# Optimization experiments

Measured on AMD Instinct MI355X. Metric: run time of the kernel, lower is better.

The kernel has to match this reference:

```python
import jax, jax.numpy as jnp
import numpy as np
import math

C = 512
B, T = 8, 2048
STRIDE = 2
LN_EPS = 1e-5
EPS = 1e-8


def _ln(x, g, b):
    mu = jnp.mean(x, axis=-1, keepdims=True)
    var = jnp.mean(jnp.square(x - mu), axis=-1, keepdims=True)
    return (x - mu) * jax.lax.rsqrt(var + LN_EPS) * g + b


def _lin(x, w, b):
    # torch Linear: y = x @ W^T + b, W: [out, in]
    return jnp.einsum('btc,oc->bto', x, w) + b


def setup_inputs() -> dict:
    key = jax.random.key(0)
    ks = iter(jax.random.split(key, 40))
    s = 0.02
    d = {'x': jax.random.normal(next(ks), (B, T, C), jnp.float32)}
    # downsample conv: [C_out, C_in, K]
    d['dw'] = jax.random.normal(next(ks), (C, C, 3), jnp.float32) * s
    d['db'] = jnp.zeros((C,), jnp.float32)
    for br in ('cr', 'd', 'c'):
        for p in ('q', 'k', 'v'):
            d[f'w{p}_{br}'] = jax.random.normal(next(ks), (C, C), jnp.float32) * s
            d[f'b{p}_{br}'] = jnp.zeros((C,), jnp.float32)
        d[f'ln_{br}_g'] = jnp.ones((C,), jnp.float32)
        d[f'ln_{br}_b'] = jnp.zeros((C,), jnp.float32)
    d['temp'] = jnp.asarray(0.1, jnp.float32)
    d['gw'] = jax.random.normal(next(ks), (3, 3 * C), jnp.float32) * s  # conv1d k=1 squeezed
    d['gb'] = jnp.zeros((3,), jnp.float32)
    return d


def _forward(x, dw, db, wq_cr, bq_cr, wk_cr, bk_cr, wv_cr, bv_cr, ln_cr_g, ln_cr_b,
             wq_d, bq_d, wk_d, bk_d, wv_d, bv_d, ln_d_g, ln_d_b,
             wq_c, bq_c, wk_c, bk_c, wv_c, bv_c, ln_c_g, ln_c_b,
             temp, gw, gb):
    scale = 1.0 / math.sqrt(C)
    # downsample: Conv1d(k=3, stride, pad=1) on [B,C,T]
    xc = jnp.transpose(x, (0, 2, 1))
    xd = jax.lax.conv_general_dilated(
        xc, dw, window_strides=(STRIDE,), padding=[(1, 1)],
        dimension_numbers=('NCH', 'OIH', 'NCH')) + db[None, :, None]
    x_down = jnp.transpose(xd, (0, 2, 1))  # [B, T//2, C]

    # cross-resolution branch
    q = _lin(x, wq_cr, bq_cr)
    k = _lin(x_down, wk_cr, bk_cr)
    v = _lin(x_down, wv_cr, bv_cr)
    a = jax.nn.softmax(jnp.einsum('btc,bsc->bts', q, k) * scale, axis=-1)
    out_cross = _ln(jnp.einsum('bts,bsc->btc', a, v), ln_cr_g, ln_cr_b)

    # dot-product branch
    q = _lin(x, wq_d, bq_d)
    k = _lin(x, wk_d, bk_d)
    v = _lin(x, wv_d, bv_d)
    a = jax.nn.softmax(jnp.einsum('btc,bsc->bts', q, k) * scale, axis=-1)
    out_dot = _ln(jnp.einsum('bts,bsc->btc', a, v), ln_d_g, ln_d_b)

    # cosine branch with learnable temperature
    q = _lin(x, wq_c, bq_c)
    k = _lin(x, wk_c, bk_c)
    qn = q / (jnp.linalg.norm(q, axis=2, keepdims=True) + EPS)
    kn = k / (jnp.linalg.norm(k, axis=2, keepdims=True) + EPS)
    t = jnp.maximum(temp, 0.01)
    a = jax.nn.softmax(jnp.einsum('btc,bsc->bts', qn, kn) / t, axis=-1)
    v = _lin(x, wv_c, bv_c)
    out_cos = _ln(jnp.einsum('bts,bsc->btc', a, v), ln_c_g, ln_c_b)

    # learned gating fusion (conv1d k=1 == per-position linear over 3C)
    fused = jnp.concatenate([out_cross, out_dot, out_cos], axis=-1)  # [B,T,3C]
    gate = jax.nn.softmax(jnp.einsum('btc,gc->btg', fused, gw) + gb, axis=-1)  # [B,T,3]
    z = (gate[..., 0:1] * out_cross + gate[..., 1:2] * out_dot + gate[..., 2:3] * out_cos)
    return z


def reference(x, dw, db, wq_cr, bq_cr, wk_cr, bk_cr, wv_cr, bv_cr, ln_cr_g, ln_cr_b,
              wq_d, bq_d, wk_d, bk_d, wv_d, bv_d, ln_d_g, ln_d_b,
              wq_c, bq_c, wk_c, bk_c, wv_c, bv_c, ln_c_g, ln_c_b,
              temp, gw, gb):
    return _forward(x, dw, db, wq_cr, bq_cr, wk_cr, bk_cr, wv_cr, bv_cr, ln_cr_g, ln_cr_b,
                    wq_d, bq_d, wk_d, bk_d, wv_d, bv_d, ln_d_g, ln_d_b,
                    wq_c, bq_c, wk_c, bk_c, wv_c, bv_c, ln_c_g, ln_c_b,
                    temp, gw, gb)
```

## Files before the change

### kernel.cpp

```cpp
#include <hip/hip_runtime.h>


typedef __attribute__((ext_vector_type(8))) __bf16 bf16x8;
typedef __attribute__((ext_vector_type(4))) float f32x4;

#define CDIM 512
#define TFULL 2048

#define GLL16(gp, lp)                                                        \
  __builtin_amdgcn_global_load_lds(                                          \
      (const __attribute__((address_space(1))) unsigned int*)(gp),           \
      (__attribute__((address_space(3))) unsigned int*)(lp), 16, 0, 0)

__device__ __forceinline__ unsigned short f2bf(float f) {
  unsigned u = __float_as_uint(f);
  u = (u + 0x7fffu + ((u >> 16) & 1u)) >> 16;
  return (unsigned short)u;
}
__device__ __forceinline__ float bf2f(unsigned short h) {
  return __uint_as_float(((unsigned)h) << 16);
}

__global__ __launch_bounds__(256)
void k_tobf16(const float* __restrict__ src, unsigned short* __restrict__ dst, long n4) {
  long i = (long)blockIdx.x * 256 + threadIdx.x;
  if (i >= n4) return;
  float4 f = reinterpret_cast<const float4*>(src)[i];
  unsigned short o4[4] = {f2bf(f.x), f2bf(f.y), f2bf(f.z), f2bf(f.w)};
  reinterpret_cast<uint2*>(dst)[i] = *reinterpret_cast<const uint2*>(o4);
}

__global__ __launch_bounds__(256)
void k_dwreorder(const float* __restrict__ dw, unsigned short* __restrict__ dwb) {
  int idx = blockIdx.x * 256 + threadIdx.x;
  if (idx >= 512 * 1536) return;
  int o = idx / 1536, rem = idx - o * 1536;
  int k = rem >> 9, i = rem & 511;
  dwb[idx] = f2bf(dw[(o * 512 + i) * 3 + k]);
}

__global__ __launch_bounds__(256)
void k_im2col(const float* __restrict__ x, unsigned short* __restrict__ aim) {
  long idx = (long)blockIdx.x * 256 + threadIdx.x;
  if (idx >= (long)8192 * 1536 / 4) return;
  long e = idx * 4;
  int row = (int)(e / 1536);
  int col = (int)(e - (long)row * 1536);
  int b = row >> 10, t = row & 1023;
  int k = col >> 9, i = col & 511;
  int r = 2 * t - 1 + k;
  float4 f = {0.f, 0.f, 0.f, 0.f};
  if (r >= 0) f = *reinterpret_cast<const float4*>(x + ((long)b * TFULL + r) * CDIM + i);
  unsigned short o4[4] = {f2bf(f.x), f2bf(f.y), f2bf(f.z), f2bf(f.w)};
  *reinterpret_cast<uint2*>(aim + e) = *reinterpret_cast<const uint2*>(o4);
}

__global__ __launch_bounds__(256)
void k_gemm(const unsigned short* __restrict__ A,
            const unsigned short* __restrict__ B,
            void* __restrict__ Cp,
            int K, int lda, int ldb, int ldc,
            long sA, long sB, long sC,
            const float* __restrict__ bias,
            float alpha, const float* __restrict__ tempPtr,
            int mode, int ldct) {
  const int gx = gridDim.x;
  const int nwg = gx * gridDim.y;
  int wg = blockIdx.x + gx * blockIdx.y;
  wg = (wg & 7) * (nwg >> 3) + (wg >> 3);
  const int tm0 = (wg % gx) * 128, tn0 = (wg / gx) * 128;
  const int bz = blockIdx.z;
  const unsigned short* Ag = A + (long)bz * sA;
  const unsigned short* Bg = B + (long)bz * sB;

  __shared__ __align__(16) unsigned short smem[32768];

  const int tid = threadIdx.x;
  const int lane = tid & 63;
  const int wave = tid >> 6;
  const int wm = (wave >> 1) * 64, wn = (wave & 1) * 64;
  const int lrow = lane & 15, kq = lane >> 4;

  f32x4 acc[4][4];
#pragma unroll
  for (int i = 0; i < 4; ++i)
#pragma unroll
    for (int j = 0; j < 4; ++j) acc[i][j] = f32x4{0.f, 0.f, 0.f, 0.f};

  const int sr = tid >> 3;
  const int sj = (tid & 7) ^ (sr & 7);
  const unsigned short* aSrc = Ag + (long)(tm0 + sr) * lda + sj * 8;
  const unsigned short* bSrc = Bg + (long)(tn0 + sr) * ldb + sj * 8;

  const int nt = K >> 6;

#define STAGE(kt_, buf_)                                                     \
  {                                                                          \
    unsigned short* aD = smem + (buf_) * 8192 + wave * 512;                  \
    unsigned short* bD = smem + 16384 + (buf_) * 8192 + wave * 512;          \
    _Pragma("unroll")                                                        \
    for (int rd = 0; rd < 4; ++rd) {                                         \
      GLL16(aSrc + (kt_) + (long)rd * 32 * lda, aD + rd * 2048);             \
      GLL16(bSrc + (kt_) + (long)rd * 32 * ldb, bD + rd * 2048);             \
    }                                                                        \
  }

  STAGE(0, 0);

  const int xr = (lrow & 7) << 3;
  for (int t = 0; t < nt; ++t) {
    __syncthreads();
    if (t + 1 < nt) STAGE((t + 1) << 6, (t + 1) & 1);
    const unsigned short* As_ = smem + (t & 1) * 8192;
    const unsigned short* Bs_ = smem + 16384 + (t & 1) * 8192;
    bf16x8 af[4][2], bfv[4][2];
#pragma unroll
    for (int mi = 0; mi < 4; ++mi)
#pragma unroll
      for (int ks = 0; ks < 2; ++ks)
        af[mi][ks] = *reinterpret_cast<const bf16x8*>(
            &As_[(wm + mi * 16 + lrow) * 64 + ((ks * 32 + kq * 8) ^ xr)]);
#pragma unroll
    for (int ni = 0; ni < 4; ++ni)
#pragma unroll
      for (int ks = 0; ks < 2; ++ks)
        bfv[ni][ks] = *reinterpret_cast<const bf16x8*>(
            &Bs_[(wn + ni * 16 + lrow) * 64 + ((ks * 32 + kq * 8) ^ xr)]);
#pragma unroll
    for (int mi = 0; mi < 4; ++mi)
#pragma unroll
      for (int ni = 0; ni < 4; ++ni) {
        acc[mi][ni] = __builtin_amdgcn_mfma_f32_16x16x32_bf16(af[mi][0], bfv[ni][0], acc[mi][ni], 0, 0, 0);
        acc[mi][ni] = __builtin_amdgcn_mfma_f32_16x16x32_bf16(af[mi][1], bfv[ni][1], acc[mi][ni], 0, 0, 0);
      }
  }
#undef STAGE

  if (tempPtr) alpha = 1.0f / fmaxf(*tempPtr, 0.01f);

  if (mode == 1) {
    unsigned short* Cb = (unsigned short*)Cp + (long)bz * sC;
#pragma unroll
    for (int mi = 0; mi < 4; ++mi) {
      int rg = tm0 + wm + mi * 16 + kq * 4;
#pragma unroll
      for (int ni = 0; ni < 4; ++ni) {
        int cg = tn0 + wn + ni * 16 + lrow;
        float bb = bias ? bias[cg] : 0.f;
        f32x4 v = acc[mi][ni];
#pragma unroll
        for (int r = 0; r < 4; ++r)
          Cb[(long)(rg + r) * ldc + cg] = f2bf(v[r] * alpha + bb);
      }
    }
  } else {
    unsigned short* Cb = (unsigned short*)Cp + (long)bz * sC;
#pragma unroll
    for (int mi = 0; mi < 4; ++mi) {
      int rg = tm0 + wm + mi * 16 + kq * 4;
#pragma unroll
      for (int ni = 0; ni < 4; ++ni) {
        int cg = tn0 + wn + ni * 16 + lrow;
        float bb = bias ? bias[cg] : 0.f;
        f32x4 v = acc[mi][ni];
#pragma unroll
        for (int r = 0; r < 4; ++r)
          Cb[(long)cg * ldct + (rg + r)] = f2bf(v[r] * alpha + bb);
      }
    }
  }
}

__global__ __launch_bounds__(256)
void k_softmax(unsigned short* __restrict__ S, int cols) {
  const long base = (long)blockIdx.x * cols;
  const int tid = threadIdx.x, lane = tid & 63, wave = tid >> 6;
  const int nv = cols >> 3;
  float f[8];
  float mx = -3.0e38f;
  if (tid < nv) {
    uint4 v = *reinterpret_cast<const uint4*>(S + base + tid * 8);
    const unsigned short* pv = (const unsigned short*)&v;
#pragma unroll
    for (int j = 0; j < 8; ++j) { f[j] = bf2f(pv[j]); mx = fmaxf(mx, f[j]); }
  }
  __shared__ float rmax[4], rsum[4];
#pragma unroll
  for (int o = 32; o > 0; o >>= 1) mx = fmaxf(mx, __shfl_down(mx, o));
  if (lane == 0) rmax[wave] = mx;
  __syncthreads();
  mx = fmaxf(fmaxf(rmax[0], rmax[1]), fmaxf(rmax[2], rmax[3]));
  float sum = 0.f;
  if (tid < nv) {
#pragma unroll
    for (int j = 0; j < 8; ++j) { f[j] = __expf(f[j] - mx); sum += f[j]; }
  }
#pragma unroll
  for (int o = 32; o > 0; o >>= 1) sum += __shfl_down(sum, o);
  if (lane == 0) rsum[wave] = sum;
  __syncthreads();
  const float inv = 1.0f / (rsum[0] + rsum[1] + rsum[2] + rsum[3]);
  if (tid < nv) {
    unsigned short o8[8];
#pragma unroll
    for (int j = 0; j < 8; ++j) o8[j] = f2bf(f[j] * inv);
    *reinterpret_cast<uint4*>(S + base + tid * 8) = *reinterpret_cast<const uint4*>(o8);
  }
}

__global__ __launch_bounds__(256)
void k_l2norm(unsigned short* __restrict__ Q) {
  const int lane = threadIdx.x & 63, wave = threadIdx.x >> 6;
  const long row = (long)blockIdx.x * 4 + wave;
  unsigned short* p = Q + row * CDIM + lane * 8;
  uint4 v = *reinterpret_cast<const uint4*>(p);
  const unsigned short* pv = (const unsigned short*)&v;
  float f[8]; float q = 0.f;
#pragma unroll
  for (int j = 0; j < 8; ++j) { f[j] = bf2f(pv[j]); q += f[j] * f[j]; }
#pragma unroll
  for (int o = 32; o > 0; o >>= 1) q += __shfl_xor(q, o);
  float sc = 1.0f / (sqrtf(q) + 1e-8f);
  unsigned short o8[8];
#pragma unroll
  for (int j = 0; j < 8; ++j) o8[j] = f2bf(f[j] * sc);
  *reinterpret_cast<uint4*>(p) = *reinterpret_cast<const uint4*>(o8);
}

__global__ __launch_bounds__(256)
void k_ln_bf(unsigned short* __restrict__ X, const float* __restrict__ g,
             const float* __restrict__ b) {
  const int lane = threadIdx.x & 63, wave = threadIdx.x >> 6;
  const long row = (long)blockIdx.x * 4 + wave;
  unsigned short* p = X + row * CDIM + lane * 8;
  uint4 v = *reinterpret_cast<const uint4*>(p);
  const unsigned short* pv = (const unsigned short*)&v;
  float f[8];
  float s = 0.f, q = 0.f;
#pragma unroll
  for (int j = 0; j < 8; ++j) { f[j] = bf2f(pv[j]); s += f[j]; q += f[j] * f[j]; }
#pragma unroll
  for (int o = 32; o > 0; o >>= 1) { s += __shfl_xor(s, o); q += __shfl_xor(q, o); }
  float mu = s * (1.f / 512.f);
  float var = q * (1.f / 512.f) - mu * mu;
  float rs = rsqrtf(var + 1e-5f);
  float gg[8], bb[8];
  *reinterpret_cast<float4*>(&gg[0]) = *reinterpret_cast<const float4*>(g + lane * 8);
  *reinterpret_cast<float4*>(&gg[4]) = *reinterpret_cast<const float4*>(g + lane * 8 + 4);
  *reinterpret_cast<float4*>(&bb[0]) = *reinterpret_cast<const float4*>(b + lane * 8);
  *reinterpret_cast<float4*>(&bb[4]) = *reinterpret_cast<const float4*>(b + lane * 8 + 4);
  unsigned short o8[8];
#pragma unroll
  for (int j = 0; j < 8; ++j) o8[j] = f2bf((f[j] - mu) * rs * gg[j] + bb[j]);
  *reinterpret_cast<uint4*>(p) = *reinterpret_cast<const uint4*>(o8);
}

__global__ __launch_bounds__(256)
void k_gate(const unsigned short* __restrict__ o0, const unsigned short* __restrict__ o1,
            const unsigned short* __restrict__ o2, const float* __restrict__ gw,
            const float* __restrict__ gb, float* __restrict__ out) {
  __shared__ float gws[3 * 1536];
  for (int i = threadIdx.x; i < 3 * 1536; i += 256) gws[i] = gw[i];
  __syncthreads();
  const int lane = threadIdx.x & 63, wave = threadIdx.x >> 6;
  const long pos = (long)blockIdx.x * 4 + wave;
  const long off = pos * CDIM + lane * 8;
  float a[8], bq[8], cq[8];
  {
    uint4 va = *reinterpret_cast<const uint4*>(o0 + off);
    uint4 vb = *reinterpret_cast<const uint4*>(o1 + off);
    uint4 vc = *reinterpret_cast<const uint4*>(o2 + off);
    const unsigned short* pa = (const unsigned short*)&va;
    const unsigned short* pb = (const unsigned short*)&vb;
    const unsigned short* pc = (const unsigned short*)&vc;
#pragma unroll
    for (int j = 0; j < 8; ++j) { a[j] = bf2f(pa[j]); bq[j] = bf2f(pb[j]); cq[j] = bf2f(pc[j]); }
  }
  float l0 = 0.f, l1 = 0.f, l2 = 0.f;
  const int ch = lane * 8;
#pragma unroll
  for (int j = 0; j < 8; ++j) {
    l0 += a[j] * gws[ch + j] + bq[j] * gws[512 + ch + j] + cq[j] * gws[1024 + ch + j];
    l1 += a[j] * gws[1536 + ch + j] + bq[j] * gws[2048 + ch + j] + cq[j] * gws[2560 + ch + j];
    l2 += a[j] * gws[3072 + ch + j] + bq[j] * gws[3584 + ch + j] + cq[j] * gws[4096 + ch + j];
  }
#pragma unroll
  for (int o = 32; o > 0; o >>= 1) {
    l0 += __shfl_xor(l0, o); l1 += __shfl_xor(l1, o); l2 += __shfl_xor(l2, o);
  }
  l0 += gb[0]; l1 += gb[1]; l2 += gb[2];
  float m = fmaxf(l0, fmaxf(l1, l2));
  float e0 = __expf(l0 - m), e1 = __expf(l1 - m), e2 = __expf(l2 - m);
  float inv = 1.f / (e0 + e1 + e2);
  float g0 = e0 * inv, g1 = e1 * inv, g2 = e2 * inv;
  float r[8];
#pragma unroll
  for (int j = 0; j < 8; ++j) r[j] = g0 * a[j] + g1 * bq[j] + g2 * cq[j];
  *reinterpret_cast<float4*>(out + off) = *reinterpret_cast<const float4*>(&r[0]);
  *reinterpret_cast<float4*>(out + off + 4) = *reinterpret_cast<const float4*>(&r[4]);
}

extern "C" void kernel_launch(void* const* d_in, const int* in_sizes, int n_in,
                              void* d_out, int out_size, void* d_ws, size_t ws_size,
                              hipStream_t stream) {
  (void)in_sizes; (void)n_in; (void)out_size;
  const float* x = (const float*)d_in[0];
  const float* dw = (const float*)d_in[1];
  const float* db = (const float*)d_in[2];
  const float* W[9] = {(const float*)d_in[3],  (const float*)d_in[5],  (const float*)d_in[7],
                       (const float*)d_in[11], (const float*)d_in[13], (const float*)d_in[15],
                       (const float*)d_in[19], (const float*)d_in[21], (const float*)d_in[23]};
  const float* bq_cr = (const float*)d_in[4];
  const float* bk_cr = (const float*)d_in[6];
  const float* bv_cr = (const float*)d_in[8];
  const float* ln_cr_g = (const float*)d_in[9];
  const float* ln_cr_b = (const float*)d_in[10];
  const float* bq_d = (const float*)d_in[12];
  const float* bk_d = (const float*)d_in[14];
  const float* bv_d = (const float*)d_in[16];
  const float* ln_d_g = (const float*)d_in[17];
  const float* ln_d_b = (const float*)d_in[18];
  const float* bq_c = (const float*)d_in[20];
  const float* bk_c = (const float*)d_in[22];
  const float* bv_c = (const float*)d_in[24];
  const float* ln_c_g = (const float*)d_in[25];
  const float* ln_c_b = (const float*)d_in[26];
  const float* temp = (const float*)d_in[27];
  const float* gw = (const float*)d_in[28];
  const float* gb = (const float*)d_in[29];

  if (ws_size < 230000000ULL) return;

  char* p = (char*)d_ws;
  auto alloc = [&](size_t bytes) {
    void* r = (void*)p;
    p += (bytes + 255) & ~(size_t)255;
    return r;
  };
  unsigned short* XB  = (unsigned short*)alloc(16384L * 512 * 2);
  unsigned short* XD  = (unsigned short*)alloc(8192L * 512 * 2);
  unsigned short* WB  = (unsigned short*)alloc(9L * 262144 * 2);
  unsigned short* DWB = (unsigned short*)alloc(512L * 1536 * 2);
  unsigned short* QB  = (unsigned short*)alloc(16384L * 512 * 2);
  unsigned short* KB  = (unsigned short*)alloc(16384L * 512 * 2);
  unsigned short* VTB = (unsigned short*)alloc(16384L * 512 * 2);
  unsigned short* OUT0 = (unsigned short*)alloc(16384L * 512 * 2);
  unsigned short* OUT1 = (unsigned short*)alloc(16384L * 512 * 2);
  unsigned short* OUT2 = (unsigned short*)alloc(16384L * 512 * 2);
  unsigned short* SB = (unsigned short*)alloc(8L * 2048 * 2048 * 2);
  unsigned short* AIM = SB;

  const float scale = 0.044194173824159216f;

  auto gemm = [&](const unsigned short* A, const unsigned short* Bm, void* Cm,
                  int M, int N, int K, int lda, int ldb, int ldc,
                  int batch, long sA, long sB, long sC,
                  const float* bias, float alpha, const float* tp, int mode, int ldct) {
    dim3 g(M / 128, N / 128, batch);
    k_gemm<<<g, 256, 0, stream>>>(A, Bm, Cm, K, lda, ldb, ldc, sA, sB, sC,
                                  bias, alpha, tp, mode, ldct);
  };

  k_tobf16<<<8192, 256, 0, stream>>>(x, XB, 16384L * 512 / 4);
  for (int j = 0; j < 9; ++j)
    k_tobf16<<<256, 256, 0, stream>>>(W[j], WB + j * 262144L, 65536);
  k_dwreorder<<<3072, 256, 0, stream>>>(dw, DWB);
  k_im2col<<<12288, 256, 0, stream>>>(x, AIM);

  gemm(AIM, DWB, XD, 8192, 512, 1536, 1536, 1536, 512, 1, 0, 0, 0,
       db, 1.f, nullptr, 1, 0);

  gemm(XB, WB + 0 * 262144L, QB, 16384, 512, 512, 512, 512, 512, 1, 0, 0, 0,
       bq_cr, 1.f, nullptr, 1, 0);
  gemm(XD, WB + 1 * 262144L, KB, 8192, 512, 512, 512, 512, 512, 1, 0, 0, 0,
       bk_cr, 1.f, nullptr, 1, 0);
  gemm(XD, WB + 2 * 262144L, VTB, 1024, 512, 512, 512, 512, 0, 8,
       1024L * 512, 0, 512L * 1024, bv_cr, 1.f, nullptr, 2, 1024);
  gemm(QB, KB, SB, 2048, 1024, 512, 512, 512, 1024, 8,
       2048L * 512, 1024L * 512, 2048L * 1024, nullptr, scale, nullptr, 1, 0);
  k_softmax<<<16384, 256, 0, stream>>>(SB, 1024);
  gemm(SB, VTB, OUT0, 2048, 512, 1024, 1024, 1024, 512, 8,
       2048L * 1024, 512L * 1024, 2048L * 512, nullptr, 1.f, nullptr, 1, 0);
  k_ln_bf<<<4096, 256, 0, stream>>>(OUT0, ln_cr_g, ln_cr_b);

  gemm(XB, WB + 3 * 262144L, QB, 16384, 512, 512, 512, 512, 512, 1, 0, 0, 0,
       bq_d, 1.f, nullptr, 1, 0);
  gemm(XB, WB + 4 * 262144L, KB, 16384, 512, 512, 512, 512, 512, 1, 0, 0, 0,
       bk_d, 1.f, nullptr, 1, 0);
  gemm(XB, WB + 5 * 262144L, VTB, 2048, 512, 512, 512, 512, 0, 8,
       2048L * 512, 0, 512L * 2048, bv_d, 1.f, nullptr, 2, 2048);
  gemm(QB, KB, SB, 2048, 2048, 512, 512, 512, 2048, 8,
       2048L * 512, 2048L * 512, 2048L * 2048, nullptr, scale, nullptr, 1, 0);
  k_softmax<<<16384, 256, 0, stream>>>(SB, 2048);
  gemm(SB, VTB, OUT1, 2048, 512, 2048, 2048, 2048, 512, 8,
       2048L * 2048, 512L * 2048, 2048L * 512, nullptr, 1.f, nullptr, 1, 0);
  k_ln_bf<<<4096, 256, 0, stream>>>(OUT1, ln_d_g, ln_d_b);

  gemm(XB, WB + 6 * 262144L, QB, 16384, 512, 512, 512, 512, 512, 1, 0, 0, 0,
       bq_c, 1.f, nullptr, 1, 0);
  gemm(XB, WB + 7 * 262144L, KB, 16384, 512, 512, 512, 512, 512, 1, 0, 0, 0,
       bk_c, 1.f, nullptr, 1, 0);
  k_l2norm<<<4096, 256, 0, stream>>>(QB);
  k_l2norm<<<4096, 256, 0, stream>>>(KB);
  gemm(XB, WB + 8 * 262144L, VTB, 2048, 512, 512, 512, 512, 0, 8,
       2048L * 512, 0, 512L * 2048, bv_c, 1.f, nullptr, 2, 2048);
  gemm(QB, KB, SB, 2048, 2048, 512, 512, 512, 2048, 8,
       2048L * 512, 2048L * 512, 2048L * 2048, nullptr, 1.f, temp, 1, 0);
  k_softmax<<<16384, 256, 0, stream>>>(SB, 2048);
  gemm(SB, VTB, OUT2, 2048, 512, 2048, 2048, 2048, 512, 8,
       2048L * 2048, 512L * 2048, 2048L * 512, nullptr, 1.f, nullptr, 1, 0);
  k_ln_bf<<<4096, 256, 0, stream>>>(OUT2, ln_c_g, ln_c_b);

  k_gate<<<4096, 256, 0, stream>>>(OUT0, OUT1, OUT2, gw, gb, (float*)d_out);
}
```

Measured before the change: 596.6 us.

## Add 256x256 GEMM for attention scores, fuse Q/K projections, batch weight casts

Adds a 512-thread GEMM kernel with 256x256 tiles, double-buffered direct-to-LDS loads and a workgroup swizzle, and uses it for the three QK^T score GEMMs. The Q and K projections of the dot and cosine branches are merged into one N=1024 GEMM that writes an interleaved QK buffer, with the biases packed by device copies. The nine weight bf16 conversions become a single launch. The aim is higher MFMA utilisation and less launch overhead, at the cost of a larger workspace, strided Q/K reads, and more register pressure in the new kernel.

```diff
diff --git a/kernel.cpp b/kernel.cpp
--- a/kernel.cpp
+++ b/kernel.cpp
@@ -28,6 +28,17 @@
   float4 f = reinterpret_cast<const float4*>(src)[i];
   unsigned short o4[4] = {f2bf(f.x), f2bf(f.y), f2bf(f.z), f2bf(f.w)};
   reinterpret_cast<uint2*>(dst)[i] = *reinterpret_cast<const uint2*>(o4);
+}
+
+struct WPtrs { const float* p[9]; };
+__global__ __launch_bounds__(256)
+void k_tobf16w(WPtrs w, unsigned short* __restrict__ dst) {
+  int idx = blockIdx.x * 256 + threadIdx.x;
+  if (idx >= 9 * 65536) return;
+  int m = idx >> 16, off = idx & 65535;
+  float4 f = reinterpret_cast<const float4*>(w.p[m])[off];
+  unsigned short o4[4] = {f2bf(f.x), f2bf(f.y), f2bf(f.z), f2bf(f.w)};
+  reinterpret_cast<uint2*>(dst + (long)m * 262144)[off] = *reinterpret_cast<const uint2*>(o4);
 }
 
 __global__ __launch_bounds__(256)
@@ -171,6 +182,103 @@
   }
 }
 
+__global__ __launch_bounds__(512)
+void k_gemm256(const unsigned short* __restrict__ A,
+               const unsigned short* __restrict__ B,
+               unsigned short* __restrict__ C,
+               int K, int lda, int ldb, int ldc,
+               long sA, long sB, long sC,
+               float alpha, const float* __restrict__ tempPtr) {
+  const int gx = gridDim.x;
+  const int nwg = gx * gridDim.y;
+  int wg = blockIdx.x + gx * blockIdx.y;
+  wg = (wg & 7) * (nwg >> 3) + (wg >> 3);
+  const int tm0 = (wg % gx) * 256, tn0 = (wg / gx) * 256;
+  const unsigned short* Ag = A + (long)blockIdx.z * sA;
+  const unsigned short* Bg = B + (long)blockIdx.z * sB;
+
+  __shared__ __align__(16) unsigned short smem[32768];
+
+  const int tid = threadIdx.x;
+  const int lane = tid & 63;
+  const int wave = tid >> 6;
+  const int wm = (wave >> 2) * 128, wn = (wave & 3) * 64;
+  const int lrow = lane & 15, kq = lane >> 4;
+
+  f32x4 acc[8][4];
+#pragma unroll
+  for (int i = 0; i < 8; ++i)
+#pragma unroll
+    for (int j = 0; j < 4; ++j) acc[i][j] = f32x4{0.f, 0.f, 0.f, 0.f};
+
+  const int srow = lane >> 2;
+  const int sslot = (lane & 3) ^ ((lane >> 3) & 3);
+  const unsigned short* aS0 = Ag + (long)(tm0 + wave * 16 + srow) * lda + sslot * 8;
+  const unsigned short* aS1 = aS0 + 128L * lda;
+  const unsigned short* bS0 = Bg + (long)(tn0 + wave * 16 + srow) * ldb + sslot * 8;
+  const unsigned short* bS1 = bS0 + 128L * ldb;
+
+  const int nt = K >> 5;
+
+#define STAGE256(kt_, buf_)                                                  \
+  {                                                                          \
+    unsigned short* aD = smem + (buf_) * 8192 + wave * 512;                  \
+    unsigned short* bD = smem + 16384 + (buf_) * 8192 + wave * 512;          \
+    GLL16(aS0 + (kt_), aD);                                                  \
+    GLL16(aS1 + (kt_), aD + 4096);                                           \
+    GLL16(bS0 + (kt_), bD);                                                  \
+    GLL16(bS1 + (kt_), bD + 4096);                                           \
+  }
+
+  STAGE256(0, 0);
+
+  const int xr = ((lrow >> 1) & 3) << 3;
+  for (int t = 0; t < nt; ++t) {
+    if (t + 1 < nt) {
+      STAGE256((t + 1) << 5, (t + 1) & 1);
+      asm volatile("s_waitcnt vmcnt(4)" ::: "memory");
+    } else {
+      asm volatile("s_waitcnt vmcnt(0)" ::: "memory");
+    }
+    __builtin_amdgcn_s_barrier();
+    __builtin_amdgcn_sched_barrier(0);
+    const unsigned short* As_ = smem + (t & 1) * 8192;
+    const unsigned short* Bs_ = smem + 16384 + (t & 1) * 8192;
+    bf16x8 bfv[4];
+#pragma unroll
+    for (int ni = 0; ni < 4; ++ni)
+      bfv[ni] = *reinterpret_cast<const bf16x8*>(
+          &Bs_[(wn + ni * 16 + lrow) * 32 + ((kq * 8) ^ xr)]);
+#pragma unroll
+    for (int mi = 0; mi < 8; ++mi) {
+      bf16x8 af = *reinterpret_cast<const bf16x8*>(
+          &As_[(wm + mi * 16 + lrow) * 32 + ((kq * 8) ^ xr)]);
+#pragma unroll
+      for (int ni = 0; ni < 4; ++ni)
+        acc[mi][ni] = __builtin_amdgcn_mfma_f32_16x16x32_bf16(af, bfv[ni], acc[mi][ni], 0, 0, 0);
+    }
+    __builtin_amdgcn_sched_barrier(0);
+    if (t + 1 < nt) __builtin_amdgcn_s_barrier();
+  }
+#undef STAGE256
+
+  if (tempPtr) alpha = 1.0f / fmaxf(*tempPtr, 0.01f);
+
+  C += (long)blockIdx.z * sC;
+#pragma unroll
+  for (int mi = 0; mi < 8; ++mi) {
+    int rg = tm0 + wm + mi * 16 + kq * 4;
+#pragma unroll
+    for (int ni = 0; ni < 4; ++ni) {
+      int cg = tn0 + wn + ni * 16 + lrow;
+      f32x4 v = acc[mi][ni];
+#pragma unroll
+      for (int r = 0; r < 4; ++r)
+        C[(long)(rg + r) * ldc + cg] = f2bf(v[r] * alpha);
+    }
+  }
+}
+
 __global__ __launch_bounds__(256)
 void k_softmax(unsigned short* __restrict__ S, int cols) {
   const long base = (long)blockIdx.x * cols;
@@ -209,10 +317,10 @@
 }
 
 __global__ __launch_bounds__(256)
-void k_l2norm(unsigned short* __restrict__ Q) {
+void k_l2norm(unsigned short* __restrict__ Q, int ld) {
   const int lane = threadIdx.x & 63, wave = threadIdx.x >> 6;
   const long row = (long)blockIdx.x * 4 + wave;
-  unsigned short* p = Q + row * CDIM + lane * 8;
+  unsigned short* p = Q + row * ld + lane * 8;
   uint4 v = *reinterpret_cast<const uint4*>(p);
   const unsigned short* pv = (const unsigned short*)&v;
   float f[8]; float q = 0.f;
@@ -307,9 +415,12 @@
   const float* x = (const float*)d_in[0];
   const float* dw = (const float*)d_in[1];
   const float* db = (const float*)d_in[2];
-  const float* W[9] = {(const float*)d_in[3],  (const float*)d_in[5],  (const float*)d_in[7],
-                       (const float*)d_in[11], (const float*)d_in[13], (const float*)d_in[15],
-                       (const float*)d_in[19], (const float*)d_in[21], (const float*)d_in[23]};
+  WPtrs wp;
+  wp.p[0] = (const float*)d_in[3];  wp.p[1] = (const float*)d_in[5];
+  wp.p[2] = (const float*)d_in[7];  wp.p[3] = (const float*)d_in[11];
+  wp.p[4] = (const float*)d_in[13]; wp.p[5] = (const float*)d_in[15];
+  wp.p[6] = (const float*)d_in[19]; wp.p[7] = (const float*)d_in[21];
+  wp.p[8] = (const float*)d_in[23];
   const float* bq_cr = (const float*)d_in[4];
   const float* bk_cr = (const float*)d_in[6];
   const float* bv_cr = (const float*)d_in[8];
@@ -329,7 +440,7 @@
   const float* gw = (const float*)d_in[28];
   const float* gb = (const float*)d_in[29];
 
-  if (ws_size < 230000000ULL) return;
+  if (ws_size < 240000000ULL) return;
 
   char* p = (char*)d_ws;
   auto alloc = [&](size_t bytes) {
@@ -342,11 +453,13 @@
   unsigned short* WB  = (unsigned short*)alloc(9L * 262144 * 2);
   unsigned short* DWB = (unsigned short*)alloc(512L * 1536 * 2);
   unsigned short* QB  = (unsigned short*)alloc(16384L * 512 * 2);
-  unsigned short* KB  = (unsigned short*)alloc(16384L * 512 * 2);
+  unsigned short* KB  = (unsigned short*)alloc(8192L * 512 * 2);
   unsigned short* VTB = (unsigned short*)alloc(16384L * 512 * 2);
   unsigned short* OUT0 = (unsigned short*)alloc(16384L * 512 * 2);
   unsigned short* OUT1 = (unsigned short*)alloc(16384L * 512 * 2);
   unsigned short* OUT2 = (unsigned short*)alloc(16384L * 512 * 2);
+  unsigned short* QK2 = (unsigned short*)alloc(16384L * 1024 * 2);
+  float* BC = (float*)alloc(2048 * 4);
   unsigned short* SB = (unsigned short*)alloc(8L * 2048 * 2048 * 2);
   unsigned short* AIM = SB;
 
@@ -360,12 +473,22 @@
     k_gemm<<<g, 256, 0, stream>>>(A, Bm, Cm, K, lda, ldb, ldc, sA, sB, sC,
                                   bias, alpha, tp, mode, ldct);
   };
+  auto gemm256 = [&](const unsigned short* A, const unsigned short* Bm,
+                     unsigned short* Cm, int M, int N, int K,
+                     int lda, int ldb, int ldc, int batch,
+                     long sA, long sB, long sC, float alpha, const float* tp) {
+    dim3 g(M / 256, N / 256, batch);
+    k_gemm256<<<g, 512, 0, stream>>>(A, Bm, Cm, K, lda, ldb, ldc, sA, sB, sC, alpha, tp);
+  };
 
   k_tobf16<<<8192, 256, 0, stream>>>(x, XB, 16384L * 512 / 4);
-  for (int j = 0; j < 9; ++j)
-    k_tobf16<<<256, 256, 0, stream>>>(W[j], WB + j * 262144L, 65536);
+  k_tobf16w<<<2304, 256, 0, stream>>>(wp, WB);
   k_dwreorder<<<3072, 256, 0, stream>>>(dw, DWB);
   k_im2col<<<12288, 256, 0, stream>>>(x, AIM);
+  hipMemcpyAsync(BC,        bq_d, 512 * 4, hipMemcpyDeviceToDevice, stream);
+  hipMemcpyAsync(BC + 512,  bk_d, 512 * 4, hipMemcpyDeviceToDevice, stream);
+  hipMemcpyAsync(BC + 1024, bq_c, 512 * 4, hipMemcpyDeviceToDevice, stream);
+  hipMemcpyAsync(BC + 1536, bk_c, 512 * 4, hipMemcpyDeviceToDevice, stream);
 
   gemm(AIM, DWB, XD, 8192, 512, 1536, 1536, 1536, 512, 1, 0, 0, 0,
        db, 1.f, nullptr, 1, 0);
@@ -376,36 +499,32 @@
        bk_cr, 1.f, nullptr, 1, 0);
   gemm(XD, WB + 2 * 262144L, VTB, 1024, 512, 512, 512, 512, 0, 8,
        1024L * 512, 0, 512L * 1024, bv_cr, 1.f, nullptr, 2, 1024);
-  gemm(QB, KB, SB, 2048, 1024, 512, 512, 512, 1024, 8,
-       2048L * 512, 1024L * 512, 2048L * 1024, nullptr, scale, nullptr, 1, 0);
+  gemm256(QB, KB, SB, 2048, 1024, 512, 512, 512, 1024, 8,
+          2048L * 512, 1024L * 512, 2048L * 1024, scale, nullptr);
   k_softmax<<<16384, 256, 0, stream>>>(SB, 1024);
   gemm(SB, VTB, OUT0, 2048, 512, 1024, 1024, 1024, 512, 8,
        2048L * 1024, 512L * 1024, 2048L * 512, nullptr, 1.f, nullptr, 1, 0);
   k_ln_bf<<<4096, 256, 0, stream>>>(OUT0, ln_cr_g, ln_cr_b);
 
-  gemm(XB, WB + 3 * 262144L, QB, 16384, 512, 512, 512, 512, 512, 1, 0, 0, 0,
-       bq_d, 1.f, nullptr, 1, 0);
-  gemm(XB, WB + 4 * 262144L, KB, 16384, 512, 512, 512, 512, 512, 1, 0, 0, 0,
-       bk_d, 1.f, nullptr, 1, 0);
+  gemm(XB, WB + 3 * 262144L, QK2, 16384, 1024, 512, 512, 512, 1024, 1, 0, 0, 0,
+       BC, 1.f, nullptr, 1, 0);
   gemm(XB, WB + 5 * 262144L, VTB, 2048, 512, 512, 512, 512, 0, 8,
        2048L * 512, 0, 512L * 2048, bv_d, 1.f, nullptr, 2, 2048);
-  gemm(QB, KB, SB, 2048, 2048, 512, 512, 512, 2048, 8,
-       2048L * 512, 2048L * 512, 2048L * 2048, nullptr, scale, nullptr, 1, 0);
+  gemm256(QK2, QK2 + 512, SB, 2048, 2048, 512, 1024, 1024, 2048, 8,
+          2048L * 1024, 2048L * 1024, 2048L * 2048, scale, nullptr);
   k_softmax<<<16384, 256, 0, stream>>>(SB, 2048);
   gemm(SB, VTB, OUT1, 2048, 512, 2048, 2048, 2048, 512, 8,
        2048L * 2048, 512L * 2048, 2048L * 512, nullptr, 1.f, nullptr, 1, 0);
   k_ln_bf<<<4096, 256, 0, stream>>>(OUT1, ln_d_g, ln_d_b);
 
-  gemm(XB, WB + 6 * 262144L, QB, 16384, 512, 512, 512, 512, 512, 1, 0, 0, 0,
-       bq_c, 1.f, nullptr, 1, 0);
-  gemm(XB, WB + 7 * 262144L, KB, 16384, 512, 512, 512, 512, 512, 1, 0, 0, 0,
-       bk_c, 1.f, nullptr, 1, 0);
-  k_l2norm<<<4096, 256, 0, stream>>>(QB);
-  k_l2norm<<<4096, 256, 0, stream>>>(KB);
+  gemm(XB, WB + 6 * 262144L, QK2, 16384, 1024, 512, 512, 512, 1024, 1, 0, 0, 0,
+       BC + 1024, 1.f, nullptr, 1, 0);
+  k_l2norm<<<4096, 256, 0, stream>>>(QK2, 1024);
+  k_l2norm<<<4096, 256, 0, stream>>>(QK2 + 512, 1024);
   gemm(XB, WB + 8 * 262144L, VTB, 2048, 512, 512, 512, 512, 0, 8,
        2048L * 512, 0, 512L * 2048, bv_c, 1.f, nullptr, 2, 2048);
-  gemm(QB, KB, SB, 2048, 2048, 512, 512, 512, 2048, 8,
-       2048L * 512, 2048L * 512, 2048L * 2048, nullptr, 1.f, temp, 1, 0);
+  gemm256(QK2, QK2 + 512, SB, 2048, 2048, 512, 1024, 1024, 2048, 8,
+          2048L * 1024, 2048L * 1024, 2048L * 2048, 1.f, temp);
   k_softmax<<<16384, 256, 0, stream>>>(SB, 2048);
   gemm(SB, VTB, OUT2, 2048, 512, 2048, 2048, 2048, 512, 8,
        2048L * 2048, 512L * 2048, 2048L * 512, nullptr, 1.f, nullptr, 1, 0);
```

Result: faster. 567.2 us (-4.9%).
